# Performance work log

Measured on AMD Instinct MI355X. Metric: run time of the kernel, lower is better.

## Reference

```python
import jax, jax.numpy as jnp
import numpy as np

T, H, I, E, TOP_K = 4096, 2048, 768, 16, 2


def _pack_i2s(tern):
    # tern: int8 in {-1,0,1}, shape [..., K] with K % 4 == 0
    m = (tern + 1).astype(jnp.uint8)  # map to {0,1,2}
    m = m.reshape(*tern.shape[:-1], -1, 4)
    return (m[..., 0] | (m[..., 1] << 2) | (m[..., 2] << 4) | (m[..., 3] << 6)).astype(jnp.uint8)


def _quantize_alpha(alpha):
    # per-column alpha -> int8 with global scale (quantize_alpha_int8)
    scale = jnp.maximum(jnp.abs(alpha).max(), 1e-8) / 127.0
    q = jnp.clip(jnp.round(alpha / scale), -128, 127).astype(jnp.int8)
    return q, scale.astype(jnp.float32)


def _unpack_i2s(packed, K, alpha):
    # packed: uint8 [..., N, K//4]; alpha: [..., K] per input column
    shifts = jnp.array([0, 2, 4, 6], dtype=jnp.uint8)
    ext = (packed[..., None] >> shifts) & jnp.uint8(3)  # [..., N, K//4, 4]
    vals = ext.reshape(*packed.shape[:-1], K).astype(jnp.float32) - 1.0  # {-1,0,1}
    return vals * alpha[..., None, :]


def setup_inputs() -> dict:
    key = jax.random.key(0)
    ks = jax.random.split(key, 6)
    x = jax.random.normal(ks[0], (T, H), dtype=jnp.float32)
    router_logits = jax.random.normal(ks[1], (T, E), dtype=jnp.float32)
    tern13 = jax.random.randint(ks[2], (E, 2 * I, H), -1, 2, dtype=jnp.int8)
    tern2 = jax.random.randint(ks[3], (E, H, I), -1, 2, dtype=jnp.int8)
    a13 = jax.random.uniform(ks[4], (E, H), minval=0.01, maxval=0.05, dtype=jnp.float32)
    a2 = jax.random.uniform(ks[5], (E, I), minval=0.01, maxval=0.05, dtype=jnp.float32)
    w13_alpha_q, w13_alpha_scale = _quantize_alpha(a13)
    w2_alpha_q, w2_alpha_scale = _quantize_alpha(a2)
    return {
        "x": x,
        "router_logits": router_logits,
        "w13_packed": _pack_i2s(tern13),
        "w13_alpha_q": w13_alpha_q,
        "w13_alpha_scale": w13_alpha_scale,
        "w2_packed": _pack_i2s(tern2),
        "w2_alpha_q": w2_alpha_q,
        "w2_alpha_scale": w2_alpha_scale,
    }


def reference(x, router_logits, w13_packed, w13_alpha_q, w13_alpha_scale,
              w2_packed, w2_alpha_q, w2_alpha_scale):
    # dequant int8 alphas, then dequant 2-bit ternary weights
    a13 = w13_alpha_q.astype(jnp.float32) * w13_alpha_scale  # [E, H]
    a2 = w2_alpha_q.astype(jnp.float32) * w2_alpha_scale     # [E, I]
    w13 = _unpack_i2s(w13_packed, H, a13)  # [E, 2I, H]
    w2 = _unpack_i2s(w2_packed, I, a2)     # [E, H, I]

    # top-k routing with renormalized softmax weights
    probs = jax.nn.softmax(router_logits, axis=-1)
    topw, topi = jax.lax.top_k(probs, TOP_K)           # [T, k]
    topw = topw / topw.sum(axis=-1, keepdims=True)
    combine = jnp.sum(jax.nn.one_hot(topi, E, dtype=x.dtype) * topw[..., None], axis=1)  # [T, E]

    # grouped expert matmuls (dense dispatch over experts)
    gu = jnp.einsum('th,enh->ten', x, w13)             # [T, E, 2I]
    gate, up = jnp.split(gu, 2, axis=-1)
    act = jax.nn.silu(gate) * up                       # [T, E, I]
    down = jnp.einsum('tei,ehi->teh', act, w2)         # [T, E, H]
    return jnp.einsum('te,teh->th', combine, down)     # [T, H]
```

## Files before the change

### kernel.cpp

```cpp
#include <hip/hip_runtime.h>
#include <stdint.h>

#define T_TOK 4096
#define HDIM  2048
#define IDIM  768
#define NEXP  16
#define NPAIR (T_TOK * 2)
#define PAIR_CAP (NPAIR + 256)

typedef float f32x4 __attribute__((ext_vector_type(4)));
typedef __bf16 bf16x8 __attribute__((ext_vector_type(8)));
typedef unsigned short u16x8 __attribute__((ext_vector_type(8)));
typedef unsigned int u32;
typedef u32 u32x4 __attribute__((ext_vector_type(4)));
typedef const __attribute__((address_space(1))) u32* as1_u32p;
typedef __attribute__((address_space(3))) u32* as3_u32p;

__device__ __forceinline__ unsigned short f2bf(float f) {
  u32 u = __float_as_uint(f);
  u += 0x7FFFu + ((u >> 16) & 1u);
  return (unsigned short)(u >> 16);
}

__device__ __forceinline__ f32x4 mfma16(bf16x8 a, bf16x8 b, f32x4 c) {
  return __builtin_amdgcn_mfma_f32_16x16x32_bf16(a, b, c, 0, 0, 0);
}

__device__ __forceinline__ bf16x8 expand8(u32 w, int qshift) {
  w >>= qshift;
  const u32 t0 = w & 0x03030303u;
  const u32 h0 = __builtin_amdgcn_perm(0u, 0x003F00BFu, t0);
  const u32 l0 = __builtin_amdgcn_perm(0u, 0x00800080u, t0);
  const u32 t1 = (w >> 2) & 0x03030303u;
  const u32 h1 = __builtin_amdgcn_perm(0u, 0x003F00BFu, t1);
  const u32 l1 = __builtin_amdgcn_perm(0u, 0x00800080u, t1);
  u32x4 o;
  o[0] = __builtin_amdgcn_perm(h0, l0, 0x05010400u);
  o[1] = __builtin_amdgcn_perm(h0, l0, 0x07030602u);
  o[2] = __builtin_amdgcn_perm(h1, l1, 0x05010400u);
  o[3] = __builtin_amdgcn_perm(h1, l1, 0x07030602u);
  return __builtin_bit_cast(bf16x8, o);
}

__global__ __launch_bounds__(256) void route_kernel(
    const float* __restrict__ logits, int* __restrict__ counts,
    int* __restrict__ t2i, float* __restrict__ t2w) {
  const int t = blockIdx.x * 256 + threadIdx.x;
  if (t >= T_TOK) return;
  const float* l = logits + t * NEXP;
  float m0 = -1e30f, m1 = -1e30f;
  int i0 = 0, i1 = 0;
#pragma unroll
  for (int j = 0; j < NEXP; ++j) {
    const float v = l[j];
    if (v > m0) { m1 = m0; i1 = i0; m0 = v; i0 = j; }
    else if (v > m1) { m1 = v; i1 = j; }
  }
  const float w0 = 1.0f / (1.0f + expf(m1 - m0));
  t2i[t] = i0 | (i1 << 8);
  t2w[t] = w0;
  atomicAdd(&counts[i0], 1);
  atomicAdd(&counts[i1], 1);
}

__global__ void scan_kernel(const int* __restrict__ counts,
                            int* __restrict__ offs, int* __restrict__ cursor) {
  if (threadIdx.x == 0) {
    int s = 0;
    for (int e = 0; e < NEXP; ++e) { offs[e] = s; cursor[e] = s; s += counts[e]; }
    offs[NEXP] = s;
  }
}

__global__ __launch_bounds__(256) void fill_kernel(
    const int* __restrict__ t2i, const float* __restrict__ t2w,
    int* __restrict__ cursor, int* __restrict__ pair_token,
    float* __restrict__ pair_wt, int* __restrict__ pair_eid,
    int* __restrict__ t2p0, int* __restrict__ t2p1) {
  const int t = blockIdx.x * 256 + threadIdx.x;
  if (t >= T_TOK) return;
  const int ii = t2i[t];
  const float w0 = t2w[t];
  const int i0 = ii & 255, i1 = (ii >> 8) & 255;
  const int p0 = atomicAdd(&cursor[i0], 1);
  pair_token[p0] = t; pair_wt[p0] = w0; pair_eid[p0] = i0;
  const int p1 = atomicAdd(&cursor[i1], 1);
  pair_token[p1] = t; pair_wt[p1] = 1.0f - w0; pair_eid[p1] = i1;
  t2p0[t] = p0; t2p1[t] = p1;
}

__global__ __launch_bounds__(256) void repack_kernel(
    const int* __restrict__ w, u32* __restrict__ o) {
  const int j0 = (blockIdx.x * 256 + threadIdx.x) * 4;
  const int4* w4 = (const int4*)w;
  uint4 r;
#pragma unroll
  for (int k = 0; k < 4; ++k) {
    const int4 a = w4[j0 + k];
    u32 x = (u32)(a.x & 255) | ((u32)(a.y & 255) << 8) |
            ((u32)(a.z & 255) << 16) | ((u32)(a.w & 255) << 24);
    u32 t = (x ^ (x >> 12)) & 0x0000F0F0u; x ^= t ^ (t << 12);
    t = (x ^ (x >> 6)) & 0x00CC00CCu;      x ^= t ^ (t << 6);
    ((u32*)&r)[k] = x;
  }
  ((uint4*)o)[blockIdx.x * 256 + threadIdx.x] = r;
}

__global__ __launch_bounds__(256) void xg_kernel(
    const float* __restrict__ x, const int* __restrict__ a13q,
    const float* __restrict__ s13p, const int* __restrict__ pair_token,
    const int* __restrict__ pair_eid, unsigned short* __restrict__ xg) {
  const int p = blockIdx.x;
  const int t = pair_token[p];
  const int e = pair_eid[p];
  const float s13 = *s13p;
  const int h0 = threadIdx.x * 8;
  const float* xp = x + (size_t)t * HDIM + h0;
  const int* ap = a13q + (size_t)e * HDIM + h0;
  const float4 x0 = ((const float4*)xp)[0];
  const float4 x1 = ((const float4*)xp)[1];
  const int4 a0 = ((const int4*)ap)[0];
  const int4 a1 = ((const int4*)ap)[1];
  u16x8 q;
  q[0] = f2bf(x0.x * (float)a0.x * s13);
  q[1] = f2bf(x0.y * (float)a0.y * s13);
  q[2] = f2bf(x0.z * (float)a0.z * s13);
  q[3] = f2bf(x0.w * (float)a0.w * s13);
  q[4] = f2bf(x1.x * (float)a1.x * s13);
  q[5] = f2bf(x1.y * (float)a1.y * s13);
  q[6] = f2bf(x1.z * (float)a1.z * s13);
  q[7] = f2bf(x1.w * (float)a1.w * s13);
  *(u16x8*)(xg + (size_t)p * HDIM + h0) = q;
}

#define DMA_A(src, pitch, dst0, dst1, sidx)                                          \
  {                                                                                  \
    _Pragma("unroll") for (int c = 0; c < 2; ++c) {                                  \
      const unsigned short* gp =                                                     \
          src + (arow0 + wave * 32 + c * 16 + arow) * (pitch) + (sidx) * 64 + acol;  \
      unsigned short* lp = dst0 + (wave * 32 + c * 16) * 32;                         \
      __builtin_amdgcn_global_load_lds((as1_u32p)(const void*)gp,                    \
                                       (as3_u32p)(void*)lp, 16, 0, 0);               \
    }                                                                                \
    _Pragma("unroll") for (int c = 0; c < 2; ++c) {                                  \
      const unsigned short* gp =                                                     \
          src + (arow0 + wave * 32 + c * 16 + arow) * (pitch) + (sidx) * 64 + 32 +   \
          acol;                                                                      \
      unsigned short* lp = dst1 + (wave * 32 + c * 16) * 32;                         \
      __builtin_amdgcn_global_load_lds((as1_u32p)(const void*)gp,                    \
                                       (as3_u32p)(void*)lp, 16, 0, 0);               \
    }                                                                                \
  }

#define LOADW(W0, W1, W2, W3, sidx)            \
  {                                            \
    W0 = *(const uint4*)(rp0 + (sidx) * 4);    \
    W1 = *(const uint4*)(rp1 + (sidx) * 4);    \
    W2 = *(const uint4*)(rp2 + (sidx) * 4);    \
    W3 = *(const uint4*)(rp3 + (sidx) * 4);    \
  }

#define MKFRAGS(fr, W0, W1, W2, W3)                       \
  {                                                       \
    fr[0] = expand8(qsel ? W0.y : W0.x, qshift);          \
    fr[1] = expand8(qsel ? W1.y : W1.x, qshift);          \
    fr[2] = expand8(qsel ? W2.y : W2.x, qshift);          \
    fr[3] = expand8(qsel ? W3.y : W3.x, qshift);          \
    fr[4] = expand8(qsel ? W0.w : W0.z, qshift);          \
    fr[5] = expand8(qsel ? W1.w : W1.z, qshift);          \
    fr[6] = expand8(qsel ? W2.w : W2.z, qshift);          \
    fr[7] = expand8(qsel ? W3.w : W3.z, qshift);          \
  }

#define MFMA4(sAx, b0, b1, b2, b3)                                                  \
  {                                                                                 \
    bf16x8 af[4];                                                                   \
    _Pragma("unroll") for (int mi = 0; mi < 4; ++mi)                                \
        af[mi] = *(const bf16x8*)(sAx + (wm * 64 + mi * 16 + ln) * 32 + quad * 8);  \
    _Pragma("unroll") for (int mi = 0; mi < 4; ++mi) {                              \
      acc[mi][0] = mfma16(af[mi], b0, acc[mi][0]);                                  \
      acc[mi][1] = mfma16(af[mi], b1, acc[mi][1]);                                  \
      acc[mi][2] = mfma16(af[mi], b2, acc[mi][2]);                                  \
      acc[mi][3] = mfma16(af[mi], b3, acc[mi][3]);                                  \
    }                                                                               \
  }

__global__ __launch_bounds__(256, 3) void gemm1_kernel(
    const u32* __restrict__ wq13, const int* __restrict__ a2q,
    const float* __restrict__ s2p, const int* __restrict__ counts,
    const int* __restrict__ offs, const float* __restrict__ pair_wt,
    const unsigned short* __restrict__ xg, unsigned short* __restrict__ act) {
  const int id = blockIdx.x;
  const int xcd = id & 7, sblk = id >> 3;
  const int nT = sblk % 12;
  const int gg = (sblk / 12) * 8 + xcd;
  const int e = gg & 15, mT = gg >> 4;
  const int cnt = counts[e];
  if (mT * 128 >= cnt) return;
  const int base = offs[e];
  const int tid = threadIdx.x;

  __shared__ __align__(16) unsigned short sA[2][2][128 * 32];

  const int wave = tid >> 6, lane = tid & 63;
  const int wm = wave >> 1, wn = wave & 1;
  const int quad = lane >> 4, ln = lane & 15;
  const int qsel = quad >> 1;
  const int qshift = (quad & 1) * 4;

  const size_t rstride = HDIM / 16;
  const u32* rp0 = wq13 + ((size_t)e * (2 * IDIM) + nT * 64 + wn * 32 + ln) * rstride;
  const u32* rp1 = rp0 + 16 * rstride;
  const u32* rp2 = rp0 + (size_t)IDIM * rstride;
  const u32* rp3 = rp2 + 16 * rstride;

  const int arow = lane >> 2;
  const int acol = (lane & 3) * 8;
  const size_t arow0 = (size_t)(base + mT * 128);

  f32x4 acc[4][4] = {};

  DMA_A(xg, HDIM, sA[0][0], sA[0][1], 0);
  uint4 WA0, WA1, WA2, WA3, WB0, WB1, WB2, WB3;
  LOADW(WA0, WA1, WA2, WA3, 0);
  LOADW(WB0, WB1, WB2, WB3, 1);

  const int S2 = (HDIM / 64) / 2;
  for (int s2 = 0; s2 < S2; ++s2) {
    const int s = 2 * s2;
    {
      bf16x8 fr[8];
      MKFRAGS(fr, WA0, WA1, WA2, WA3);
      __syncthreads();
      DMA_A(xg, HDIM, sA[1][0], sA[1][1], s + 1);
      if (s2 + 1 < S2) LOADW(WA0, WA1, WA2, WA3, s + 2);
      __builtin_amdgcn_s_setprio(1);
      MFMA4(sA[0][0], fr[0], fr[1], fr[2], fr[3]);
      MFMA4(sA[0][1], fr[4], fr[5], fr[6], fr[7]);
      __builtin_amdgcn_s_setprio(0);
    }
    {
      bf16x8 fr[8];
      MKFRAGS(fr, WB0, WB1, WB2, WB3);
      __syncthreads();
      if (s2 + 1 < S2) {
        DMA_A(xg, HDIM, sA[0][0], sA[0][1], s + 2);
        LOADW(WB0, WB1, WB2, WB3, s + 3);
      }
      __builtin_amdgcn_s_setprio(1);
      MFMA4(sA[1][0], fr[0], fr[1], fr[2], fr[3]);
      MFMA4(sA[1][1], fr[4], fr[5], fr[6], fr[7]);
      __builtin_amdgcn_s_setprio(0);
    }
  }

  const float s2v = *s2p;
#pragma unroll
  for (int gi = 0; gi < 2; ++gi) {
    const int i = nT * 64 + wn * 32 + gi * 16 + ln;
    const float a2v = (float)a2q[e * IDIM + i] * s2v;
#pragma unroll
    for (int mi = 0; mi < 4; ++mi) {
      const f32x4 g = acc[mi][gi];
      const f32x4 u = acc[mi][gi + 2];
#pragma unroll
      for (int r = 0; r < 4; ++r) {
        const int m = mT * 128 + wm * 64 + mi * 16 + quad * 4 + r;
        if (m < cnt) {
          const float wt = pair_wt[base + m];
          const float gv = g[r];
          const float av = gv / (1.0f + __expf(-gv)) * u[r] * a2v * wt;
          act[(size_t)(base + m) * IDIM + i] = f2bf(av);
        }
      }
    }
  }
}

__global__ __launch_bounds__(256, 3) void gemm2_kernel(
    const u32* __restrict__ wq2, const int* __restrict__ counts,
    const int* __restrict__ offs, const unsigned short* __restrict__ act,
    unsigned short* __restrict__ down) {
  const int id = blockIdx.x;
  const int xcd = id & 7, sblk = id >> 3;
  const int nT = sblk & 15;
  const int gg = (sblk >> 4) * 8 + xcd;
  const int e = gg & 15, mT = gg >> 4;
  const int cnt = counts[e];
  if (mT * 128 >= cnt) return;
  const int base = offs[e];
  const int tid = threadIdx.x;

  __shared__ __align__(16) unsigned short sA[2][2][128 * 32];

  const int wave = tid >> 6, lane = tid & 63;
  const int wm = wave >> 1, wn = wave & 1;
  const int quad = lane >> 4, ln = lane & 15;
  const int qsel = quad >> 1;
  const int qshift = (quad & 1) * 4;

  const size_t rstride = IDIM / 16;
  const u32* rp0 = wq2 + ((size_t)e * HDIM + nT * 128 + wn * 64 + ln) * rstride;
  const u32* rp1 = rp0 + 16 * rstride;
  const u32* rp2 = rp0 + 32 * rstride;
  const u32* rp3 = rp0 + 48 * rstride;

  const int arow = lane >> 2;
  const int acol = (lane & 3) * 8;
  const size_t arow0 = (size_t)(base + mT * 128);

  f32x4 acc[4][4] = {};

  DMA_A(act, IDIM, sA[0][0], sA[0][1], 0);
  uint4 WA0, WA1, WA2, WA3, WB0, WB1, WB2, WB3;
  LOADW(WA0, WA1, WA2, WA3, 0);
  LOADW(WB0, WB1, WB2, WB3, 1);

  const int S2 = (IDIM / 64) / 2;
  for (int s2 = 0; s2 < S2; ++s2) {
    const int s = 2 * s2;
    {
      bf16x8 fr[8];
      MKFRAGS(fr, WA0, WA1, WA2, WA3);
      __syncthreads();
      DMA_A(act, IDIM, sA[1][0], sA[1][1], s + 1);
      if (s2 + 1 < S2) LOADW(WA0, WA1, WA2, WA3, s + 2);
      __builtin_amdgcn_s_setprio(1);
      MFMA4(sA[0][0], fr[0], fr[1], fr[2], fr[3]);
      MFMA4(sA[0][1], fr[4], fr[5], fr[6], fr[7]);
      __builtin_amdgcn_s_setprio(0);
    }
    {
      bf16x8 fr[8];
      MKFRAGS(fr, WB0, WB1, WB2, WB3);
      __syncthreads();
      if (s2 + 1 < S2) {
        DMA_A(act, IDIM, sA[0][0], sA[0][1], s + 2);
        LOADW(WB0, WB1, WB2, WB3, s + 3);
      }
      __builtin_amdgcn_s_setprio(1);
      MFMA4(sA[1][0], fr[0], fr[1], fr[2], fr[3]);
      MFMA4(sA[1][1], fr[4], fr[5], fr[6], fr[7]);
      __builtin_amdgcn_s_setprio(0);
    }
  }

#pragma unroll
  for (int mi = 0; mi < 4; ++mi) {
#pragma unroll
    for (int r = 0; r < 4; ++r) {
      const int ml = wm * 64 + mi * 16 + quad * 4 + r;
      const int m = mT * 128 + ml;
      if (m < cnt) {
        unsigned short* drow = down + (size_t)(base + m) * HDIM + nT * 128 + wn * 64;
#pragma unroll
        for (int ni = 0; ni < 4; ++ni)
          drow[ni * 16 + ln] = f2bf(acc[mi][ni][r]);
      }
    }
  }
}

__global__ __launch_bounds__(256) void combine_kernel(
    const int* __restrict__ t2p0, const int* __restrict__ t2p1,
    const unsigned short* __restrict__ down, float* __restrict__ out) {
  const int t = blockIdx.x;
  const int h = threadIdx.x * 8;
  const u16x8 a = *(const u16x8*)(down + (size_t)t2p0[t] * HDIM + h);
  const u16x8 b = *(const u16x8*)(down + (size_t)t2p1[t] * HDIM + h);
  f32x4 o0, o1;
#pragma unroll
  for (int j = 0; j < 4; ++j) {
    o0[j] = __uint_as_float((u32)a[j] << 16) + __uint_as_float((u32)b[j] << 16);
    o1[j] = __uint_as_float((u32)a[j + 4] << 16) + __uint_as_float((u32)b[j + 4] << 16);
  }
  float* o = out + (size_t)t * HDIM + h;
  *(f32x4*)(o) = o0;
  *(f32x4*)(o + 4) = o1;
}

extern "C" void kernel_launch(void* const* d_in, const int* in_sizes, int n_in,
                              void* d_out, int out_size, void* d_ws, size_t ws_size,
                              hipStream_t stream) {
  const float* x      = (const float*)d_in[0];
  const float* logits = (const float*)d_in[1];
  const int*   w13p   = (const int*)d_in[2];
  const int*   a13q   = (const int*)d_in[3];
  const float* s13    = (const float*)d_in[4];
  const int*   w2p    = (const int*)d_in[5];
  const int*   a2q    = (const int*)d_in[6];
  const float* s2     = (const float*)d_in[7];
  float* out = (float*)d_out;

  char* ws = (char*)d_ws;
  int*   counts     = (int*)(ws + 0);
  int*   cursor     = (int*)(ws + 64);
  int*   offs       = (int*)(ws + 128);
  int*   t2i        = (int*)(ws + 256);
  float* t2w        = (float*)(ws + 256 + 4 * T_TOK);
  int*   t2p0       = (int*)(ws + 256 + 8 * T_TOK);
  int*   t2p1       = (int*)(ws + 256 + 12 * T_TOK);
  int*   pair_token = (int*)(ws + 256 + 16 * T_TOK);
  float* pair_wt    = (float*)(ws + 256 + 16 * T_TOK + 4 * PAIR_CAP);
  int*   pair_eid   = (int*)(ws + 256 + 16 * T_TOK + 8 * PAIR_CAP);
  const size_t hdr_end = ((size_t)(256 + 16 * T_TOK + 12 * PAIR_CAP) + 255) & ~(size_t)255;

  const size_t n32_13 = (size_t)NEXP * 2 * IDIM * (HDIM / 16);
  const size_t n32_2  = (size_t)NEXP * HDIM * (IDIM / 16);
  const size_t rp13_b = n32_13 * 4, rp2_b = n32_2 * 4;
  const size_t xg_b   = (size_t)PAIR_CAP * HDIM * 2;

  u32* rp13 = (u32*)(ws + hdr_end);
  u32* rp2  = (u32*)(ws + hdr_end + rp13_b);
  unsigned short* xg  = (unsigned short*)(ws + hdr_end + rp13_b + rp2_b);
  unsigned short* act = (unsigned short*)(ws + hdr_end + rp13_b + rp2_b + xg_b);
  unsigned short* down = xg;

  hipMemsetAsync(counts, 0, 256, stream);
  route_kernel<<<T_TOK / 256, 256, 0, stream>>>(logits, counts, t2i, t2w);
  scan_kernel<<<1, 64, 0, stream>>>(counts, offs, cursor);
  fill_kernel<<<T_TOK / 256, 256, 0, stream>>>(t2i, t2w, cursor, pair_token, pair_wt,
                                               pair_eid, t2p0, t2p1);
  repack_kernel<<<(int)(n32_13 / 1024), 256, 0, stream>>>(w13p, rp13);
  repack_kernel<<<(int)(n32_2 / 1024), 256, 0, stream>>>(w2p, rp2);
  xg_kernel<<<NPAIR, 256, 0, stream>>>(x, a13q, s13, pair_token, pair_eid, xg);

  gemm1_kernel<<<6144, 256, 0, stream>>>(rp13, a2q, s2, counts, offs, pair_wt, xg, act);
  gemm2_kernel<<<8192, 256, 0, stream>>>(rp2, counts, offs, act, down);
  combine_kernel<<<T_TOK, 256, 0, stream>>>(t2p0, t2p1, down, out);
}
```

Before: 386.7 us.

## Stage packed weight tiles in LDS via async DMA instead of register prefetch

Packed ternary weight tiles for both expert GEMMs now go into double-buffered LDS through global_load_lds issued by two waves, instead of each wave holding register-prefetched uint4 weights. Each wave reads its u32 words from LDS and expands them just before the MFMAs. Dropping the eight uint4 prefetch registers lets launch bounds rise from 3 to 4 blocks per CU for more occupancy. The cost is extra LDS reads per half-step and the expand now sitting on the critical path after the barrier.

```diff
diff --git a/kernel.cpp b/kernel.cpp
--- a/kernel.cpp
+++ b/kernel.cpp
@@ -152,31 +152,35 @@
     }                                                                                \
   }
 
-#define LOADW(W0, W1, W2, W3, sidx)            \
-  {                                            \
-    W0 = *(const uint4*)(rp0 + (sidx) * 4);    \
-    W1 = *(const uint4*)(rp1 + (sidx) * 4);    \
-    W2 = *(const uint4*)(rp2 + (sidx) * 4);    \
-    W3 = *(const uint4*)(rp3 + (sidx) * 4);    \
-  }
-
-#define MKFRAGS(fr, W0, W1, W2, W3)                       \
-  {                                                       \
-    fr[0] = expand8(qsel ? W0.y : W0.x, qshift);          \
-    fr[1] = expand8(qsel ? W1.y : W1.x, qshift);          \
-    fr[2] = expand8(qsel ? W2.y : W2.x, qshift);          \
-    fr[3] = expand8(qsel ? W3.y : W3.x, qshift);          \
-    fr[4] = expand8(qsel ? W0.w : W0.z, qshift);          \
-    fr[5] = expand8(qsel ? W1.w : W1.z, qshift);          \
-    fr[6] = expand8(qsel ? W2.w : W2.z, qshift);          \
-    fr[7] = expand8(qsel ? W3.w : W3.z, qshift);          \
-  }
-
-#define MFMA4(sAx, b0, b1, b2, b3)                                                  \
+#define DMA_B1(dstq, sidx)                                                           \
+  if (wave < 2) {                                                                    \
+    const u32* gq = wq13 + ((size_t)e * (2 * IDIM) + wave * IDIM + nT * 64 + lane) * \
+                               (HDIM / 16) + (size_t)(sidx) * 4;                     \
+    u32* lp = (dstq) + wave * 256;                                                   \
+    __builtin_amdgcn_global_load_lds((as1_u32p)(const void*)gq,                      \
+                                     (as3_u32p)(void*)lp, 16, 0, 0);                 \
+  }
+
+#define DMA_B2(dstq, sidx)                                                           \
+  if (wave < 2) {                                                                    \
+    const u32* gq = wq2 + ((size_t)e * HDIM + nT * 128 + wave * 64 + lane) *         \
+                              (IDIM / 16) + (size_t)(sidx) * 4;                      \
+    u32* lp = (dstq) + wave * 256;                                                   \
+    __builtin_amdgcn_global_load_lds((as1_u32p)(const void*)gq,                      \
+                                     (as3_u32p)(void*)lp, 16, 0, 0);                 \
+  }
+
+#define G1_HALF(sAp, sBp, h)                                                        \
   {                                                                                 \
     bf16x8 af[4];                                                                   \
     _Pragma("unroll") for (int mi = 0; mi < 4; ++mi)                                \
-        af[mi] = *(const bf16x8*)(sAx + (wm * 64 + mi * 16 + ln) * 32 + quad * 8);  \
+        af[mi] = *(const bf16x8*)((sAp) + (wm * 64 + mi * 16 + ln) * 32 + quad * 8);\
+    const u32 c0 = (sBp)[(wn * 32 + ln) * 4 + 2 * (h) + qsel];                      \
+    const u32 c1 = (sBp)[(wn * 32 + 16 + ln) * 4 + 2 * (h) + qsel];                 \
+    const u32 c2 = (sBp)[(64 + wn * 32 + ln) * 4 + 2 * (h) + qsel];                 \
+    const u32 c3 = (sBp)[(64 + wn * 32 + 16 + ln) * 4 + 2 * (h) + qsel];            \
+    const bf16x8 b0 = expand8(c0, qshift), b1 = expand8(c1, qshift);                \
+    const bf16x8 b2 = expand8(c2, qshift), b3 = expand8(c3, qshift);                \
     _Pragma("unroll") for (int mi = 0; mi < 4; ++mi) {                              \
       acc[mi][0] = mfma16(af[mi], b0, acc[mi][0]);                                  \
       acc[mi][1] = mfma16(af[mi], b1, acc[mi][1]);                                  \
@@ -185,7 +189,26 @@
     }                                                                               \
   }
 
-__global__ __launch_bounds__(256, 3) void gemm1_kernel(
+#define G2_HALF(sAp, sBp, h)                                                        \
+  {                                                                                 \
+    bf16x8 af[4];                                                                   \
+    _Pragma("unroll") for (int mi = 0; mi < 4; ++mi)                                \
+        af[mi] = *(const bf16x8*)((sAp) + (wm * 64 + mi * 16 + ln) * 32 + quad * 8);\
+    const u32 c0 = (sBp)[(wn * 64 + ln) * 4 + 2 * (h) + qsel];                      \
+    const u32 c1 = (sBp)[(wn * 64 + 16 + ln) * 4 + 2 * (h) + qsel];                 \
+    const u32 c2 = (sBp)[(wn * 64 + 32 + ln) * 4 + 2 * (h) + qsel];                 \
+    const u32 c3 = (sBp)[(wn * 64 + 48 + ln) * 4 + 2 * (h) + qsel];                 \
+    const bf16x8 b0 = expand8(c0, qshift), b1 = expand8(c1, qshift);                \
+    const bf16x8 b2 = expand8(c2, qshift), b3 = expand8(c3, qshift);                \
+    _Pragma("unroll") for (int mi = 0; mi < 4; ++mi) {                              \
+      acc[mi][0] = mfma16(af[mi], b0, acc[mi][0]);                                  \
+      acc[mi][1] = mfma16(af[mi], b1, acc[mi][1]);                                  \
+      acc[mi][2] = mfma16(af[mi], b2, acc[mi][2]);                                  \
+      acc[mi][3] = mfma16(af[mi], b3, acc[mi][3]);                                  \
+    }                                                                               \
+  }
+
+__global__ __launch_bounds__(256, 4) void gemm1_kernel(
     const u32* __restrict__ wq13, const int* __restrict__ a2q,
     const float* __restrict__ s2p, const int* __restrict__ counts,
     const int* __restrict__ offs, const float* __restrict__ pair_wt,
@@ -201,6 +224,7 @@
   const int tid = threadIdx.x;
 
   __shared__ __align__(16) unsigned short sA[2][2][128 * 32];
+  __shared__ __align__(16) u32 sBq[2][512];
 
   const int wave = tid >> 6, lane = tid & 63;
   const int wm = wave >> 1, wn = wave & 1;
@@ -208,12 +232,6 @@
   const int qsel = quad >> 1;
   const int qshift = (quad & 1) * 4;
 
-  const size_t rstride = HDIM / 16;
-  const u32* rp0 = wq13 + ((size_t)e * (2 * IDIM) + nT * 64 + wn * 32 + ln) * rstride;
-  const u32* rp1 = rp0 + 16 * rstride;
-  const u32* rp2 = rp0 + (size_t)IDIM * rstride;
-  const u32* rp3 = rp2 + 16 * rstride;
-
   const int arow = lane >> 2;
   const int acol = (lane & 3) * 8;
   const size_t arow0 = (size_t)(base + mT * 128);
@@ -221,37 +239,27 @@
   f32x4 acc[4][4] = {};
 
   DMA_A(xg, HDIM, sA[0][0], sA[0][1], 0);
-  uint4 WA0, WA1, WA2, WA3, WB0, WB1, WB2, WB3;
-  LOADW(WA0, WA1, WA2, WA3, 0);
-  LOADW(WB0, WB1, WB2, WB3, 1);
-
-  const int S2 = (HDIM / 64) / 2;
-  for (int s2 = 0; s2 < S2; ++s2) {
-    const int s = 2 * s2;
-    {
-      bf16x8 fr[8];
-      MKFRAGS(fr, WA0, WA1, WA2, WA3);
-      __syncthreads();
-      DMA_A(xg, HDIM, sA[1][0], sA[1][1], s + 1);
-      if (s2 + 1 < S2) LOADW(WA0, WA1, WA2, WA3, s + 2);
-      __builtin_amdgcn_s_setprio(1);
-      MFMA4(sA[0][0], fr[0], fr[1], fr[2], fr[3]);
-      MFMA4(sA[0][1], fr[4], fr[5], fr[6], fr[7]);
-      __builtin_amdgcn_s_setprio(0);
+  DMA_B1(sBq[0], 0);
+
+  const int NT = HDIM / 64;
+  for (int j2 = 0; j2 < NT / 2; ++j2) {
+    const int j = 2 * j2;
+    __syncthreads();
+    DMA_A(xg, HDIM, sA[1][0], sA[1][1], j + 1);
+    DMA_B1(sBq[1], j + 1);
+    __builtin_amdgcn_s_setprio(1);
+    G1_HALF(sA[0][0], sBq[0], 0);
+    G1_HALF(sA[0][1], sBq[0], 1);
+    __builtin_amdgcn_s_setprio(0);
+    __syncthreads();
+    if (j2 + 1 < NT / 2) {
+      DMA_A(xg, HDIM, sA[0][0], sA[0][1], j + 2);
+      DMA_B1(sBq[0], j + 2);
     }
-    {
-      bf16x8 fr[8];
-      MKFRAGS(fr, WB0, WB1, WB2, WB3);
-      __syncthreads();
-      if (s2 + 1 < S2) {
-        DMA_A(xg, HDIM, sA[0][0], sA[0][1], s + 2);
-        LOADW(WB0, WB1, WB2, WB3, s + 3);
-      }
-      __builtin_amdgcn_s_setprio(1);
-      MFMA4(sA[1][0], fr[0], fr[1], fr[2], fr[3]);
-      MFMA4(sA[1][1], fr[4], fr[5], fr[6], fr[7]);
-      __builtin_amdgcn_s_setprio(0);
-    }
+    __builtin_amdgcn_s_setprio(1);
+    G1_HALF(sA[1][0], sBq[1], 0);
+    G1_HALF(sA[1][1], sBq[1], 1);
+    __builtin_amdgcn_s_setprio(0);
   }
 
   const float s2v = *s2p;
@@ -277,7 +285,7 @@
   }
 }
 
-__global__ __launch_bounds__(256, 3) void gemm2_kernel(
+__global__ __launch_bounds__(256, 4) void gemm2_kernel(
     const u32* __restrict__ wq2, const int* __restrict__ counts,
     const int* __restrict__ offs, const unsigned short* __restrict__ act,
     unsigned short* __restrict__ down) {
@@ -292,6 +300,7 @@
   const int tid = threadIdx.x;
 
   __shared__ __align__(16) unsigned short sA[2][2][128 * 32];
+  __shared__ __align__(16) u32 sBq[2][512];
 
   const int wave = tid >> 6, lane = tid & 63;
   const int wm = wave >> 1, wn = wave & 1;
@@ -299,12 +308,6 @@
   const int qsel = quad >> 1;
   const int qshift = (quad & 1) * 4;
 
-  const size_t rstride = IDIM / 16;
-  const u32* rp0 = wq2 + ((size_t)e * HDIM + nT * 128 + wn * 64 + ln) * rstride;
-  const u32* rp1 = rp0 + 16 * rstride;
-  const u32* rp2 = rp0 + 32 * rstride;
-  const u32* rp3 = rp0 + 48 * rstride;
-
   const int arow = lane >> 2;
   const int acol = (lane & 3) * 8;
   const size_t arow0 = (size_t)(base + mT * 128);
@@ -312,37 +315,27 @@
   f32x4 acc[4][4] = {};
 
   DMA_A(act, IDIM, sA[0][0], sA[0][1], 0);
-  uint4 WA0, WA1, WA2, WA3, WB0, WB1, WB2, WB3;
-  LOADW(WA0, WA1, WA2, WA3, 0);
-  LOADW(WB0, WB1, WB2, WB3, 1);
-
-  const int S2 = (IDIM / 64) / 2;
-  for (int s2 = 0; s2 < S2; ++s2) {
-    const int s = 2 * s2;
-    {
-      bf16x8 fr[8];
-      MKFRAGS(fr, WA0, WA1, WA2, WA3);
-      __syncthreads();
-      DMA_A(act, IDIM, sA[1][0], sA[1][1], s + 1);
-      if (s2 + 1 < S2) LOADW(WA0, WA1, WA2, WA3, s + 2);
-      __builtin_amdgcn_s_setprio(1);
-      MFMA4(sA[0][0], fr[0], fr[1], fr[2], fr[3]);
-      MFMA4(sA[0][1], fr[4], fr[5], fr[6], fr[7]);
-      __builtin_amdgcn_s_setprio(0);
+  DMA_B2(sBq[0], 0);
+
+  const int NT = IDIM / 64;
+  for (int j2 = 0; j2 < NT / 2; ++j2) {
+    const int j = 2 * j2;
+    __syncthreads();
+    DMA_A(act, IDIM, sA[1][0], sA[1][1], j + 1);
+    DMA_B2(sBq[1], j + 1);
+    __builtin_amdgcn_s_setprio(1);
+    G2_HALF(sA[0][0], sBq[0], 0);
+    G2_HALF(sA[0][1], sBq[0], 1);
+    __builtin_amdgcn_s_setprio(0);
+    __syncthreads();
+    if (j2 + 1 < NT / 2) {
+      DMA_A(act, IDIM, sA[0][0], sA[0][1], j + 2);
+      DMA_B2(sBq[0], j + 2);
     }
-    {
-      bf16x8 fr[8];
-      MKFRAGS(fr, WB0, WB1, WB2, WB3);
-      __syncthreads();
-      if (s2 + 1 < S2) {
-        DMA_A(act, IDIM, sA[0][0], sA[0][1], s + 2);
-        LOADW(WB0, WB1, WB2, WB3, s + 3);
-      }
-      __builtin_amdgcn_s_setprio(1);
-      MFMA4(sA[1][0], fr[0], fr[1], fr[2], fr[3]);
-      MFMA4(sA[1][1], fr[4], fr[5], fr[6], fr[7]);
-      __builtin_amdgcn_s_setprio(0);
-    }
+    __builtin_amdgcn_s_setprio(1);
+    G2_HALF(sA[1][0], sBq[1], 0);
+    G2_HALF(sA[1][1], sBq[1], 1);
+    __builtin_amdgcn_s_setprio(0);
   }
 
 #pragma unroll
```

Result: faster. 331.5 us (-14.3%).
